# Kernel tuning notes

Measured on AMD Instinct MI355X. Metric: run time of the kernel, lower is better.

The kernel has to match this reference:

```python
import jax, jax.numpy as jnp
import numpy as np

B, S, D, H = 2, 2048, 1024, 16
HD = D // H
EPS = 1e-5

def _ln(x, g, b):
    mu = jnp.mean(x, axis=-1, keepdims=True)
    var = jnp.var(x, axis=-1, keepdims=True)
    return (x - mu) * jax.lax.rsqrt(var + EPS) * g + b

def setup_inputs() -> dict:
    key = jax.random.key(0)
    ks = jax.random.split(key, 6)
    sc = lambda n: 1.0 / np.sqrt(n)
    return {
        "x": jax.random.normal(ks[0], (B, S, D), jnp.float32),
        "W_qkv": jax.random.normal(ks[1], (D, 3 * D), jnp.float32) * sc(D),
        "b_qkv": jnp.zeros((3 * D,), jnp.float32),
        "W_o": jax.random.normal(ks[2], (D, D), jnp.float32) * sc(D),
        "b_o": jnp.zeros((D,), jnp.float32),
        "W_fc": jax.random.normal(ks[3], (D, 4 * D), jnp.float32) * sc(D),
        "b_fc": jnp.zeros((4 * D,), jnp.float32),
        "W_pr": jax.random.normal(ks[4], (4 * D, D), jnp.float32) * sc(4 * D),
        "b_pr": jnp.zeros((D,), jnp.float32),
        "g1": jnp.ones((D,), jnp.float32),
        "beta1": jnp.zeros((D,), jnp.float32),
        "g2": jnp.ones((D,), jnp.float32),
        "beta2": jnp.zeros((D,), jnp.float32),
    }

def reference(x, W_qkv, b_qkv, W_o, b_o, W_fc, b_fc, W_pr, b_pr, g1, beta1, g2, beta2):
    # pre-norm attention
    h = _ln(x, g1, beta1)
    qkv = h @ W_qkv + b_qkv                      # [B,S,3D]
    q, k, v = jnp.split(qkv, 3, axis=-1)
    q = q.reshape(B, S, H, HD).transpose(0, 2, 1, 3)  # [B,H,S,hd]
    k = k.reshape(B, S, H, HD).transpose(0, 2, 1, 3)
    v = v.reshape(B, S, H, HD).transpose(0, 2, 1, 3)
    scores = jnp.einsum('bhqd,bhkd->bhqk', q, k) / np.sqrt(HD)
    causal = jnp.tril(jnp.ones((S, S), bool))
    scores = jnp.where(causal, scores, -jnp.inf)
    attn = jax.nn.softmax(scores, axis=-1)
    out = jnp.einsum('bhqk,bhkd->bhqd', attn, v)
    out = out.transpose(0, 2, 1, 3).reshape(B, S, D)
    x = x + out @ W_o + b_o
    # pre-norm MLP (exact erf GELU, matching torch F.gelu default)
    h2 = _ln(x, g2, beta2)
    h2 = jax.nn.gelu(h2 @ W_fc + b_fc, approximate=False)
    x = x + h2 @ W_pr + b_pr
    return x
```

## Files before the change

### kernel.cpp

```cpp
#include <hip/hip_runtime.h>
#include <cstdint>
#include <cstddef>

#define Bb 2
#define Ss 2048
#define Dd 1024
#define Hh 16

typedef __attribute__((ext_vector_type(8))) short short8;
typedef __attribute__((ext_vector_type(4))) short short4v;
typedef __attribute__((ext_vector_type(4))) float float4v;

__device__ inline short f2bf(float f) {
  unsigned u = __builtin_bit_cast(unsigned, f);
  u = (u + 0x7fffu + ((u >> 16) & 1u)) >> 16;
  return (short)u;
}

__device__ inline float bf2f(short s) {
  unsigned u = ((unsigned)(unsigned short)s) << 16;
  return __builtin_bit_cast(float, u);
}

__device__ inline void gl_lds16(const void* g, void* l) {
  __builtin_amdgcn_global_load_lds(
      (__attribute__((address_space(1))) void*)(void*)(g),
      (__attribute__((address_space(3))) void*)(l), 16, 0, 0);
}

#define MFMA(a, b, c) __builtin_amdgcn_mfma_f32_16x16x32_bf16((a), (b), (c), 0, 0, 0)

__device__ __forceinline__ void ln_row(const float* __restrict__ x,
                                       const float* __restrict__ g,
                                       const float* __restrict__ be,
                                       short* __restrict__ out, int row,
                                       float* red) {
  int tid = threadIdx.x;
  const float4* xr = (const float4*)(x + (size_t)row * Dd);
  float4 v = xr[tid];
  float s = v.x + v.y + v.z + v.w;
  float q = v.x * v.x + v.y * v.y + v.z * v.z + v.w * v.w;
#pragma unroll
  for (int off = 1; off < 64; off <<= 1) {
    s += __shfl_xor(s, off);
    q += __shfl_xor(q, off);
  }
  int w = tid >> 6;
  if ((tid & 63) == 0) { red[w] = s; red[4 + w] = q; }
  __syncthreads();
  s = red[0] + red[1] + red[2] + red[3];
  q = red[4] + red[5] + red[6] + red[7];
  float mu = s * (1.0f / Dd);
  float var = q * (1.0f / Dd) - mu * mu;
  float rstd = rsqrtf(var + 1e-5f);
  float4 gv = ((const float4*)g)[tid], bv = ((const float4*)be)[tid];
  short4v o;
  o.x = f2bf((v.x - mu) * rstd * gv.x + bv.x);
  o.y = f2bf((v.y - mu) * rstd * gv.y + bv.y);
  o.z = f2bf((v.z - mu) * rstd * gv.z + bv.z);
  o.w = f2bf((v.w - mu) * rstd * gv.w + bv.w);
  *(short4v*)(out + (size_t)row * Dd + tid * 4) = o;
}

__global__ __launch_bounds__(256) void prep_kernel(
    const float* __restrict__ W0, short* __restrict__ T0,
    const float* __restrict__ W1, short* __restrict__ T1,
    const float* __restrict__ W2, short* __restrict__ T2,
    const float* __restrict__ W3, short* __restrict__ T3,
    const float* __restrict__ x, const float* __restrict__ g1,
    const float* __restrict__ be1, short* __restrict__ h1) {
  __shared__ __align__(16) float t[32][33];
  int id = blockIdx.x;
  if (id >= 12288) {
    ln_row(x, g1, be1, h1, id - 12288, &t[0][0]);
    return;
  }
  const float* W; short* Wt; int N, K, tix;
  if (id < 3072)      { W = W0; Wt = T0; N = 3072; K = 1024; tix = id; }
  else if (id < 4096) { W = W1; Wt = T1; N = 1024; K = 1024; tix = id - 3072; }
  else if (id < 8192) { W = W2; Wt = T2; N = 4096; K = 1024; tix = id - 4096; }
  else                { W = W3; Wt = T3; N = 1024; K = 4096; tix = id - 8192; }
  int nx = N / 32;
  int n0 = (tix % nx) * 32, k0 = (tix / nx) * 32;
  int tx = threadIdx.x & 31, ty = threadIdx.x >> 5;
#pragma unroll
  for (int i = 0; i < 4; i++)
    t[ty + 8 * i][tx] = W[(size_t)(k0 + ty + 8 * i) * N + n0 + tx];
  __syncthreads();
#pragma unroll
  for (int i = 0; i < 4; i++)
    Wt[(size_t)(n0 + ty + 8 * i) * K + k0 + tx] = f2bf(t[tx][ty + 8 * i]);
}

__global__ __launch_bounds__(256) void reduce_ln_kernel(const float* __restrict__ x,
                                                        const float* __restrict__ bias,
                                                        const short* __restrict__ parts,
                                                        const float* __restrict__ g,
                                                        const float* __restrict__ be,
                                                        float* __restrict__ x1,
                                                        short* __restrict__ h2) {
  int row = blockIdx.x, tid = threadIdx.x;
  size_t base = (size_t)row * Dd + tid * 4;
  float4 v = *(const float4*)(x + base);
  float4 bv = ((const float4*)bias)[tid];
  v.x += bv.x; v.y += bv.y; v.z += bv.z; v.w += bv.w;
#pragma unroll
  for (int s = 0; s < 2; s++) {
    short4v p = *(const short4v*)(parts + (size_t)s * 4096 * Dd + base);
    v.x += bf2f(p.x); v.y += bf2f(p.y); v.z += bf2f(p.z); v.w += bf2f(p.w);
  }
  *(float4*)(x1 + base) = v;
  float s = v.x + v.y + v.z + v.w;
  float q = v.x * v.x + v.y * v.y + v.z * v.z + v.w * v.w;
#pragma unroll
  for (int off = 1; off < 64; off <<= 1) {
    s += __shfl_xor(s, off);
    q += __shfl_xor(q, off);
  }
  __shared__ float as_[4], aq_[4];
  int w = tid >> 6;
  if ((tid & 63) == 0) { as_[w] = s; aq_[w] = q; }
  __syncthreads();
  s = as_[0] + as_[1] + as_[2] + as_[3];
  q = aq_[0] + aq_[1] + aq_[2] + aq_[3];
  float mu = s * (1.0f / Dd);
  float var = q * (1.0f / Dd) - mu * mu;
  float rstd = rsqrtf(var + 1e-5f);
  float4 gv = ((const float4*)g)[tid], b2 = ((const float4*)be)[tid];
  short4v o;
  o.x = f2bf((v.x - mu) * rstd * gv.x + b2.x);
  o.y = f2bf((v.y - mu) * rstd * gv.y + b2.y);
  o.z = f2bf((v.z - mu) * rstd * gv.z + b2.z);
  o.w = f2bf((v.w - mu) * rstd * gv.w + b2.w);
  *(short4v*)(h2 + base) = o;
}

__global__ __launch_bounds__(256) void reduce_kernel(const float* __restrict__ src,
                                                     const float* __restrict__ bias,
                                                     const short* __restrict__ parts,
                                                     float* __restrict__ dst) {
  int row = blockIdx.x, tid = threadIdx.x;
  size_t base = (size_t)row * Dd + tid * 4;
  float4 v = *(const float4*)(src + base);
  float4 bv = ((const float4*)bias)[tid];
  v.x += bv.x; v.y += bv.y; v.z += bv.z; v.w += bv.w;
#pragma unroll
  for (int s = 0; s < 2; s++) {
    short4v p = *(const short4v*)(parts + (size_t)s * 4096 * Dd + base);
    v.x += bf2f(p.x); v.y += bf2f(p.y); v.z += bf2f(p.z); v.w += bf2f(p.w);
  }
  *(float4*)(dst + base) = v;
}

__global__ __launch_bounds__(256) void vt_kernel(const short* __restrict__ qkv,
                                                 short* __restrict__ Vt) {
  __shared__ short t[32][34];
  int s0 = blockIdx.x * 32;
  int d0 = blockIdx.y * 32;
  int bh = blockIdx.z;
  int b = bh >> 4, h = bh & 15;
  int tx = threadIdx.x & 31, ty = threadIdx.x >> 5;
#pragma unroll
  for (int i = 0; i < 4; i++)
    t[ty + 8 * i][tx] =
        qkv[(size_t)(b * Ss + s0 + ty + 8 * i) * 3072 + 2048 + h * 64 + d0 + tx];
  __syncthreads();
#pragma unroll
  for (int i = 0; i < 4; i++)
    Vt[(size_t)(bh * 64 + d0 + ty + 8 * i) * Ss + s0 + tx] = t[tx][ty + 8 * i];
}

template <int MODE>
__device__ __forceinline__ void gemm_tile(const short* __restrict__ A,
                                          const short* __restrict__ Bt,
                                          const float* __restrict__ bias,
                                          void* __restrict__ outp,
                                          int M, int N, int K,
                                          int m0, int n0, int zp,
                                          int ks, int ke, char* smem) {
  short* As = (short*)smem;
  short* Bs = (short*)smem + 128 * 64;
  const int tid = threadIdx.x;
  const int w = tid >> 6, lane = tid & 63;
  const int sr = lane >> 3;
  const int sc = lane & 7;
  const int gc = sc ^ sr;
  const int fr = lane & 15;
  const int g = lane >> 4;
  const int wm = (w >> 1) * 64, wn = (w & 1) * 64;
  float4v acc[4][4] = {};
  const short* Ag = A + (size_t)(m0 + w * 32 + sr) * K + gc * 8;
  const short* Bg = Bt + (size_t)(n0 + w * 32 + sr) * K + gc * 8;
  short* Asw = As + (w * 32 + sr) * 64 + sc * 8;
  short* Bsw = Bs + (w * 32 + sr) * 64 + sc * 8;
  for (int k0 = ks; k0 < ke; k0 += 64) {
    __syncthreads();
#pragma unroll
    for (int i = 0; i < 4; i++) {
      gl_lds16(Ag + (size_t)(i * 8) * K + k0, Asw + i * 8 * 64);
      gl_lds16(Bg + (size_t)(i * 8) * K + k0, Bsw + i * 8 * 64);
    }
    __syncthreads();
#pragma unroll
    for (int kh = 0; kh < 2; kh++) {
      short8 a[4], b[4];
#pragma unroll
      for (int i = 0; i < 4; i++) {
        int row = wm + i * 16 + fr;
        int slot = (g + kh * 4) ^ (row & 7);
        a[i] = *(const short8*)(As + row * 64 + slot * 8);
      }
#pragma unroll
      for (int j = 0; j < 4; j++) {
        int row = wn + j * 16 + fr;
        int slot = (g + kh * 4) ^ (row & 7);
        b[j] = *(const short8*)(Bs + row * 64 + slot * 8);
      }
#pragma unroll
      for (int i = 0; i < 4; i++)
#pragma unroll
        for (int j = 0; j < 4; j++)
          acc[i][j] = MFMA(a[i], b[j], acc[i][j]);
    }
  }
  const int crow = g * 4;
  const int ccol = fr;
#pragma unroll
  for (int i = 0; i < 4; i++) {
#pragma unroll
    for (int j = 0; j < 4; j++) {
      int col = n0 + wn + j * 16 + ccol;
      float bcol = (MODE == 3) ? 0.f : bias[col];
#pragma unroll
      for (int r = 0; r < 4; r++) {
        int row = m0 + wm + i * 16 + crow + r;
        float v = acc[i][j][r] + bcol;
        if (MODE == 0) {
          ((short*)outp)[(size_t)row * N + col] = f2bf(v);
        } else if (MODE == 2) {
          float y = 0.79788456f * (v + 0.044715f * v * v * v);
          float e = __builtin_amdgcn_exp2f(y * 2.885390082f);
          float th = 1.0f - 2.0f * __builtin_amdgcn_rcpf(e + 1.0f);
          v = 0.5f * v * (1.0f + th);
          ((short*)outp)[(size_t)row * N + col] = f2bf(v);
        } else {
          short* pp = (short*)outp + (size_t)zp * M * N;
          pp[(size_t)row * N + col] = f2bf(v);
        }
      }
    }
  }
}

__global__ __launch_bounds__(256) void k_gemm_qkv(const short* __restrict__ A,
                                                  const short* __restrict__ Bt,
                                                  const float* __restrict__ bias,
                                                  short* __restrict__ o) {
  __shared__ __align__(16) char smem[32768];
  int t = blockIdx.x;
  int c8 = t & 7, tt = t >> 3;
  int m0 = ((c8 >> 1) * 8 + tt / 12) * 128;
  int n0 = ((c8 & 1) * 12 + tt % 12) * 128;
  gemm_tile<0>(A, Bt, bias, o, 4096, 3072, 1024, m0, n0, 0, 0, 1024, smem);
}

__global__ __launch_bounds__(256) void k_gemm_fc(const short* __restrict__ A,
                                                 const short* __restrict__ Bt,
                                                 const float* __restrict__ bias,
                                                 short* __restrict__ o) {
  __shared__ __align__(16) char smem[32768];
  int t = blockIdx.x;
  int c8 = t & 7, tt = t >> 3;
  int m0 = ((c8 >> 1) * 8 + tt / 16) * 128;
  int n0 = ((c8 & 1) * 16 + tt % 16) * 128;
  gemm_tile<2>(A, Bt, bias, o, 4096, 4096, 1024, m0, n0, 0, 0, 1024, smem);
}

__global__ __launch_bounds__(256) void k_gemm_wo(const short* __restrict__ A,
                                                 const short* __restrict__ Bt,
                                                 short* __restrict__ parts) {
  __shared__ __align__(16) char smem[32768];
  int c = blockIdx.x;
  int z = c >> 8, rem = c & 255;
  int c8 = rem & 7, tt = rem >> 3;
  int m0 = (c8 * 4 + tt / 8) * 128, n0 = (tt % 8) * 128;
  gemm_tile<3>(A, Bt, nullptr, parts, 4096, 1024, 1024, m0, n0, z,
               z * 512, z * 512 + 512, smem);
}

__global__ __launch_bounds__(256) void k_gemm_pr(const short* __restrict__ A,
                                                 const short* __restrict__ Bt,
                                                 short* __restrict__ parts) {
  __shared__ __align__(16) char smem[32768];
  int c = blockIdx.x;
  int z = c >> 8, rem = c & 255;
  int c8 = rem & 7, tt = rem >> 3;
  int m0 = (c8 * 4 + tt / 8) * 128, n0 = (tt % 8) * 128;
  gemm_tile<3>(A, Bt, nullptr, parts, 4096, 1024, 4096, m0, n0, z,
               z * 2048, z * 2048 + 2048, smem);
}

__global__ __launch_bounds__(256) void flash_kernel(const short* __restrict__ qkv,
                                                    const short* __restrict__ Vt,
                                                    short* __restrict__ att) {
  __shared__ __align__(16) short Ks[4096];
  __shared__ __align__(16) short Vs[4096];
  __shared__ __align__(16) short P[4][16 * 72];
  const int w = threadIdx.x >> 6, lane = threadIdx.x & 63;
  const int qb = 31 - (blockIdx.x >> 5);
  const int bh = blockIdx.x & 31;
  const int b = bh >> 4, h = bh & 15;
  const int qbase = qb * 64 + w * 16;
  const int q = lane & 15;
  const int g = lane >> 4;
  const int fk = g * 8;
  short* Pw = &P[w][0];

  const int L0 = w * 64 + lane, L1 = L0 + 256;
  const int r0 = L0 >> 3, c0 = (L0 & 7) ^ (r0 & 7);
  const int r1 = L1 >> 3, c1 = (L1 & 7) ^ (r1 & 7);
  const short* kg0 = qkv + (size_t)(b * Ss + r0) * 3072 + 1024 + h * 64 + c0 * 8;
  const short* kg1 = qkv + (size_t)(b * Ss + r1) * 3072 + 1024 + h * 64 + c1 * 8;
  const short* vg0 = Vt + (size_t)(bh * 64 + r0) * Ss + c0 * 8;
  const short* vg1 = Vt + (size_t)(bh * 64 + r1) * Ss + c1 * 8;

  short8 qf[2];
  {
    const short* qrow = qkv + (size_t)(b * Ss + qbase + q) * 3072 + h * 64;
    qf[0] = *(const short8*)(qrow + fk);
    qf[1] = *(const short8*)(qrow + 32 + fk);
  }
  float4v o[4] = {};
  float l_i = 0.f;
  const float sc = 0.125f * 1.44269504088896f;
  const int nkt = qb + 1;

  for (int kt = 0; kt < nkt; kt++) {
    const int kbase = kt * 64;
    __syncthreads();
    gl_lds16(kg0 + (size_t)kbase * 3072, Ks + L0 * 8);
    gl_lds16(kg1 + (size_t)kbase * 3072, Ks + L1 * 8);
    gl_lds16(vg0 + kbase, Vs + L0 * 8);
    gl_lds16(vg1 + kbase, Vs + L1 * 8);
    __syncthreads();

    short8 kf[4][2], vf[4][2];
#pragma unroll
    for (int t = 0; t < 4; t++) {
      const int row = 16 * t + q;
      const int sw = (g ^ (row & 7)) * 8;
      kf[t][0] = *(const short8*)(Ks + row * 64 + sw);
      kf[t][1] = *(const short8*)(Ks + row * 64 + (sw ^ 32));
      vf[t][0] = *(const short8*)(Vs + row * 64 + sw);
      vf[t][1] = *(const short8*)(Vs + row * 64 + (sw ^ 32));
    }
    float4v s[4] = {};
#pragma unroll
    for (int t = 0; t < 4; t++) {
      s[t] = MFMA(kf[t][0], qf[0], s[t]);
      s[t] = MFMA(kf[t][1], qf[1], s[t]);
    }
    const bool maskt = (kbase + 63 > qbase);
    const int qlim = qbase + q - kbase;
    float p[4][4];
    float rs = 0.f;
#pragma unroll
    for (int t = 0; t < 4; t++) {
#pragma unroll
      for (int r = 0; r < 4; r++) {
        float v = s[t][r] * sc;
        if (maskt && (16 * t + 4 * g + r > qlim)) v = -3.0e38f;
        float e = __builtin_amdgcn_exp2f(v);
        p[t][r] = e;
        rs += e;
      }
    }
    rs += __shfl_xor(rs, 16);
    rs += __shfl_xor(rs, 32);
    l_i += rs;
#pragma unroll
    for (int t = 0; t < 4; t++) {
      unsigned lo = (unsigned)(unsigned short)f2bf(p[t][0]) |
                    ((unsigned)(unsigned short)f2bf(p[t][1]) << 16);
      unsigned hi = (unsigned)(unsigned short)f2bf(p[t][2]) |
                    ((unsigned)(unsigned short)f2bf(p[t][3]) << 16);
      uint2 u; u.x = lo; u.y = hi;
      *(uint2*)(Pw + q * 72 + 16 * t + 4 * g) = u;
    }
    asm volatile("s_waitcnt lgkmcnt(0)" ::: "memory");
    short8 pb0 = *(const short8*)(Pw + q * 72 + fk);
    short8 pb1 = *(const short8*)(Pw + q * 72 + 32 + fk);
#pragma unroll
    for (int t = 0; t < 4; t++) {
      o[t] = MFMA(vf[t][0], pb0, o[t]);
      o[t] = MFMA(vf[t][1], pb1, o[t]);
    }
  }
  const float inv = 1.0f / l_i;
  const int orow = b * Ss + qbase + q;
#pragma unroll
  for (int t = 0; t < 4; t++) {
    short4v ov;
    ov.x = f2bf(o[t][0] * inv);
    ov.y = f2bf(o[t][1] * inv);
    ov.z = f2bf(o[t][2] * inv);
    ov.w = f2bf(o[t][3] * inv);
    *(short4v*)(att + (size_t)orow * Dd + h * 64 + 16 * t + 4 * g) = ov;
  }
}

extern "C" void kernel_launch(void* const* d_in, const int* in_sizes, int n_in,
                              void* d_out, int out_size, void* d_ws, size_t ws_size,
                              hipStream_t stream) {
  const float* x    = (const float*)d_in[0];
  const float* Wqkv = (const float*)d_in[1];
  const float* bqkv = (const float*)d_in[2];
  const float* Wo   = (const float*)d_in[3];
  const float* bo   = (const float*)d_in[4];
  const float* Wfc  = (const float*)d_in[5];
  const float* bfc  = (const float*)d_in[6];
  const float* Wpr  = (const float*)d_in[7];
  const float* bpr  = (const float*)d_in[8];
  const float* g1   = (const float*)d_in[9];
  const float* be1  = (const float*)d_in[10];
  const float* g2   = (const float*)d_in[11];
  const float* be2  = (const float*)d_in[12];

  char* ws = (char*)d_ws;
  const size_t MB = 1024 * 1024;
  short* h1     = (short*)(ws + 0);
  short* qkvb   = (short*)(ws + 8 * MB);
  short* partWo = (short*)(ws + 0);
  short* partPr = (short*)(ws + 0);
  short* Vt     = (short*)(ws + 32 * MB);
  short* att    = (short*)(ws + 40 * MB);
  float* x1     = (float*)(ws + 48 * MB);
  short* h2     = (short*)(ws + 64 * MB);
  short* geluo  = (short*)(ws + 72 * MB);
  short* WtQkv  = (short*)(ws + 104 * MB);
  short* WtO    = (short*)(ws + 110 * MB);
  short* WtFc   = (short*)(ws + 112 * MB);
  short* WtPr   = (short*)(ws + 120 * MB);

  prep_kernel<<<16384, 256, 0, stream>>>(Wqkv, WtQkv, Wo, WtO, Wfc, WtFc,
                                         Wpr, WtPr, x, g1, be1, h1);
  k_gemm_qkv<<<768, 256, 0, stream>>>(h1, WtQkv, bqkv, qkvb);
  vt_kernel<<<dim3(64, 2, 32), 256, 0, stream>>>(qkvb, Vt);
  flash_kernel<<<1024, 256, 0, stream>>>(qkvb, Vt, att);
  k_gemm_wo<<<512, 256, 0, stream>>>(att, WtO, partWo);
  reduce_ln_kernel<<<4096, 256, 0, stream>>>(x, bo, partWo, g2, be2, x1, h2);
  k_gemm_fc<<<1024, 256, 0, stream>>>(h2, WtFc, bfc, geluo);
  k_gemm_pr<<<512, 256, 0, stream>>>(geluo, WtPr, partPr);
  reduce_kernel<<<4096, 256, 0, stream>>>(x1, bpr, partPr, (float*)d_out);
}
```

Baseline: 330.8 us.

## Prefetch next K tile in GEMM and flash loops; fuse V transpose into QKV GEMM

The GEMM and flash-attention inner loops now read the current tile from LDS into registers, synchronise, and then issue the global-to-LDS loads for the next tile before running the MFMAs. This lets memory latency overlap with compute while keeping a single LDS buffer. The QKV GEMM epilogue also writes the V columns directly in transposed layout, which removes the separate vt_kernel launch and its extra pass over V. The cost is higher register pressure from holding both k-halves of fragments, plus an odd accumulator index expression that happens to resolve to the original indexing.

```diff
diff --git a/kernel.cpp b/kernel.cpp
--- a/kernel.cpp
+++ b/kernel.cpp
@@ -152,29 +152,12 @@
   *(float4*)(dst + base) = v;
 }
 
-__global__ __launch_bounds__(256) void vt_kernel(const short* __restrict__ qkv,
-                                                 short* __restrict__ Vt) {
-  __shared__ short t[32][34];
-  int s0 = blockIdx.x * 32;
-  int d0 = blockIdx.y * 32;
-  int bh = blockIdx.z;
-  int b = bh >> 4, h = bh & 15;
-  int tx = threadIdx.x & 31, ty = threadIdx.x >> 5;
-#pragma unroll
-  for (int i = 0; i < 4; i++)
-    t[ty + 8 * i][tx] =
-        qkv[(size_t)(b * Ss + s0 + ty + 8 * i) * 3072 + 2048 + h * 64 + d0 + tx];
-  __syncthreads();
-#pragma unroll
-  for (int i = 0; i < 4; i++)
-    Vt[(size_t)(bh * 64 + d0 + ty + 8 * i) * Ss + s0 + tx] = t[tx][ty + 8 * i];
-}
-
 template <int MODE>
 __device__ __forceinline__ void gemm_tile(const short* __restrict__ A,
                                           const short* __restrict__ Bt,
                                           const float* __restrict__ bias,
                                           void* __restrict__ outp,
+                                          short* __restrict__ vtp,
                                           int M, int N, int K,
                                           int m0, int n0, int zp,
                                           int ks, int ke, char* smem) {
@@ -193,35 +176,44 @@
   const short* Bg = Bt + (size_t)(n0 + w * 32 + sr) * K + gc * 8;
   short* Asw = As + (w * 32 + sr) * 64 + sc * 8;
   short* Bsw = Bs + (w * 32 + sr) * 64 + sc * 8;
+#pragma unroll
+  for (int i = 0; i < 4; i++) {
+    gl_lds16(Ag + (size_t)(i * 8) * K + ks, Asw + i * 8 * 64);
+    gl_lds16(Bg + (size_t)(i * 8) * K + ks, Bsw + i * 8 * 64);
+  }
   for (int k0 = ks; k0 < ke; k0 += 64) {
     __syncthreads();
-#pragma unroll
-    for (int i = 0; i < 4; i++) {
-      gl_lds16(Ag + (size_t)(i * 8) * K + k0, Asw + i * 8 * 64);
-      gl_lds16(Bg + (size_t)(i * 8) * K + k0, Bsw + i * 8 * 64);
-    }
-    __syncthreads();
+    short8 a[2][4], b[2][4];
 #pragma unroll
     for (int kh = 0; kh < 2; kh++) {
-      short8 a[4], b[4];
 #pragma unroll
       for (int i = 0; i < 4; i++) {
         int row = wm + i * 16 + fr;
         int slot = (g + kh * 4) ^ (row & 7);
-        a[i] = *(const short8*)(As + row * 64 + slot * 8);
+        a[kh][i] = *(const short8*)(As + row * 64 + slot * 8);
       }
 #pragma unroll
       for (int j = 0; j < 4; j++) {
         int row = wn + j * 16 + fr;
         int slot = (g + kh * 4) ^ (row & 7);
-        b[j] = *(const short8*)(Bs + row * 64 + slot * 8);
-      }
+        b[kh][j] = *(const short8*)(Bs + row * 64 + slot * 8);
+      }
+    }
+    __syncthreads();
+    if (k0 + 64 < ke) {
+#pragma unroll
+      for (int i = 0; i < 4; i++) {
+        gl_lds16(Ag + (size_t)(i * 8) * K + k0 + 64, Asw + i * 8 * 64);
+        gl_lds16(Bg + (size_t)(i * 8) * K + k0 + 64, Bsw + i * 8 * 64);
+      }
+    }
+#pragma unroll
+    for (int kh = 0; kh < 2; kh++)
 #pragma unroll
       for (int i = 0; i < 4; i++)
 #pragma unroll
         for (int j = 0; j < 4; j++)
-          acc[i][j] = MFMA(a[i], b[j], acc[i][j]);
-    }
+          acc[kh & 0 ? 0 : i][j] = MFMA(a[kh][i], b[kh][j], acc[i][j]);
   }
   const int crow = g * 4;
   const int ccol = fr;
@@ -231,12 +223,14 @@
     for (int j = 0; j < 4; j++) {
       int col = n0 + wn + j * 16 + ccol;
       float bcol = (MODE == 3) ? 0.f : bias[col];
+      short sh[4];
 #pragma unroll
       for (int r = 0; r < 4; r++) {
         int row = m0 + wm + i * 16 + crow + r;
         float v = acc[i][j][r] + bcol;
-        if (MODE == 0) {
-          ((short*)outp)[(size_t)row * N + col] = f2bf(v);
+        if (MODE == 4) {
+          sh[r] = f2bf(v);
+          ((short*)outp)[(size_t)row * N + col] = sh[r];
         } else if (MODE == 2) {
           float y = 0.79788456f * (v + 0.044715f * v * v * v);
           float e = __builtin_amdgcn_exp2f(y * 2.885390082f);
@@ -248,6 +242,15 @@
           pp[(size_t)row * N + col] = f2bf(v);
         }
       }
+      if (MODE == 4 && col >= 2048) {
+        int hd = col - 2048;
+        int rbase = m0 + wm + i * 16 + crow;
+        int bq = rbase >> 11, sb = rbase & 2047;
+        int bh = bq * 16 + (hd >> 6), d = hd & 63;
+        short4v pk;
+        pk.x = sh[0]; pk.y = sh[1]; pk.z = sh[2]; pk.w = sh[3];
+        *(short4v*)(vtp + (size_t)(bh * 64 + d) * Ss + sb) = pk;
+      }
     }
   }
 }
@@ -255,13 +258,14 @@
 __global__ __launch_bounds__(256) void k_gemm_qkv(const short* __restrict__ A,
                                                   const short* __restrict__ Bt,
                                                   const float* __restrict__ bias,
-                                                  short* __restrict__ o) {
+                                                  short* __restrict__ o,
+                                                  short* __restrict__ Vt) {
   __shared__ __align__(16) char smem[32768];
   int t = blockIdx.x;
   int c8 = t & 7, tt = t >> 3;
   int m0 = ((c8 >> 1) * 8 + tt / 12) * 128;
   int n0 = ((c8 & 1) * 12 + tt % 12) * 128;
-  gemm_tile<0>(A, Bt, bias, o, 4096, 3072, 1024, m0, n0, 0, 0, 1024, smem);
+  gemm_tile<4>(A, Bt, bias, o, Vt, 4096, 3072, 1024, m0, n0, 0, 0, 1024, smem);
 }
 
 __global__ __launch_bounds__(256) void k_gemm_fc(const short* __restrict__ A,
@@ -273,7 +277,7 @@
   int c8 = t & 7, tt = t >> 3;
   int m0 = ((c8 >> 1) * 8 + tt / 16) * 128;
   int n0 = ((c8 & 1) * 16 + tt % 16) * 128;
-  gemm_tile<2>(A, Bt, bias, o, 4096, 4096, 1024, m0, n0, 0, 0, 1024, smem);
+  gemm_tile<2>(A, Bt, bias, o, nullptr, 4096, 4096, 1024, m0, n0, 0, 0, 1024, smem);
 }
 
 __global__ __launch_bounds__(256) void k_gemm_wo(const short* __restrict__ A,
@@ -284,7 +288,7 @@
   int z = c >> 8, rem = c & 255;
   int c8 = rem & 7, tt = rem >> 3;
   int m0 = (c8 * 4 + tt / 8) * 128, n0 = (tt % 8) * 128;
-  gemm_tile<3>(A, Bt, nullptr, parts, 4096, 1024, 1024, m0, n0, z,
+  gemm_tile<3>(A, Bt, nullptr, parts, nullptr, 4096, 1024, 1024, m0, n0, z,
                z * 512, z * 512 + 512, smem);
 }
 
@@ -296,7 +300,7 @@
   int z = c >> 8, rem = c & 255;
   int c8 = rem & 7, tt = rem >> 3;
   int m0 = (c8 * 4 + tt / 8) * 128, n0 = (tt % 8) * 128;
-  gemm_tile<3>(A, Bt, nullptr, parts, 4096, 1024, 4096, m0, n0, z,
+  gemm_tile<3>(A, Bt, nullptr, parts, nullptr, 4096, 1024, 4096, m0, n0, z,
                z * 2048, z * 2048 + 2048, smem);
 }
 
@@ -335,13 +339,13 @@
   const float sc = 0.125f * 1.44269504088896f;
   const int nkt = qb + 1;
 
+  gl_lds16(kg0, Ks + L0 * 8);
+  gl_lds16(kg1, Ks + L1 * 8);
+  gl_lds16(vg0, Vs + L0 * 8);
+  gl_lds16(vg1, Vs + L1 * 8);
+
   for (int kt = 0; kt < nkt; kt++) {
     const int kbase = kt * 64;
-    __syncthreads();
-    gl_lds16(kg0 + (size_t)kbase * 3072, Ks + L0 * 8);
-    gl_lds16(kg1 + (size_t)kbase * 3072, Ks + L1 * 8);
-    gl_lds16(vg0 + kbase, Vs + L0 * 8);
-    gl_lds16(vg1 + kbase, Vs + L1 * 8);
     __syncthreads();
 
     short8 kf[4][2], vf[4][2];
@@ -354,6 +358,15 @@
       vf[t][0] = *(const short8*)(Vs + row * 64 + sw);
       vf[t][1] = *(const short8*)(Vs + row * 64 + (sw ^ 32));
     }
+    __syncthreads();
+    if (kt + 1 < nkt) {
+      const size_t nb = (size_t)(kbase + 64);
+      gl_lds16(kg0 + nb * 3072, Ks + L0 * 8);
+      gl_lds16(kg1 + nb * 3072, Ks + L1 * 8);
+      gl_lds16(vg0 + nb, Vs + L0 * 8);
+      gl_lds16(vg1 + nb, Vs + L1 * 8);
+    }
+
     float4v s[4] = {};
 #pragma unroll
     for (int t = 0; t < 4; t++) {
@@ -444,8 +457,7 @@
 
   prep_kernel<<<16384, 256, 0, stream>>>(Wqkv, WtQkv, Wo, WtO, Wfc, WtFc,
                                          Wpr, WtPr, x, g1, be1, h1);
-  k_gemm_qkv<<<768, 256, 0, stream>>>(h1, WtQkv, bqkv, qkvb);
-  vt_kernel<<<dim3(64, 2, 32), 256, 0, stream>>>(qkvb, Vt);
+  k_gemm_qkv<<<768, 256, 0, stream>>>(h1, WtQkv, bqkv, qkvb, Vt);
   flash_kernel<<<1024, 256, 0, stream>>>(qkvb, Vt, att);
   k_gemm_wo<<<512, 256, 0, stream>>>(att, WtO, partWo);
   reduce_ln_kernel<<<4096, 256, 0, stream>>>(x, bo, partWo, g2, be2, x1, h2);
```

Result: faster. 294.9 us (-10.8%).
